# Kernel optimization log

Hardware: AMD Instinct MI355X
Metric: run time of the kernel (lower is better)

The kernel has to match this reference:

```python
import jax, jax.numpy as jnp
import numpy as np

B, S, E, H, DK, DV = 2, 2048, 1024, 16, 64, 64
NEG = -1e9


def setup_inputs() -> dict:
    key = jax.random.key(0)
    ks = jax.random.split(key, 12)
    s = 0.02
    return {
        "query": jax.random.normal(ks[0], (B, S, E), jnp.float32),
        "key": jax.random.normal(ks[1], (B, S, E), jnp.float32),
        "value": jax.random.normal(ks[2], (B, S, E), jnp.float32),
        "mask": jax.random.randint(ks[3], (B, S, S), 0, 2, jnp.int32),
        "Wq": jax.random.normal(ks[4], (E, H * DK), jnp.float32) * s,
        "bq": jnp.zeros((H * DK,), jnp.float32),
        "Wk": jax.random.normal(ks[5], (E, H * DK), jnp.float32) * s,
        "bk": jnp.zeros((H * DK,), jnp.float32),
        "Wv": jax.random.normal(ks[6], (E, H * DV), jnp.float32) * s,
        "bv": jnp.zeros((H * DV,), jnp.float32),
        "Wo": jax.random.normal(ks[7], (H * DV, E), jnp.float32) * s,
        "bo": jnp.zeros((E,), jnp.float32),
    }


def reference(query, key, value, mask, Wq, bq, Wk, bk, Wv, bv, Wo, bo):
    # projections, then split heads: (B,S,H*D) -> (B,H,S,D)
    q = (query @ Wq + bq).reshape(B, S, H, DK).transpose(0, 2, 1, 3)
    k = (key @ Wk + bk).reshape(B, S, H, DK).transpose(0, 2, 1, 3)
    v = (value @ Wv + bv).reshape(B, S, H, DV).transpose(0, 2, 1, 3)
    scores = jnp.einsum("bhqd,bhkd->bhqk", q, k) / jnp.sqrt(jnp.float32(DK))
    scores = jnp.where(mask[:, None, :, :] == 0, jnp.float32(NEG), scores)
    weights = jax.nn.softmax(scores, axis=-1)
    ctx = jnp.einsum("bhqk,bhkd->bhqd", weights, v)
    ctx = ctx.transpose(0, 2, 1, 3).reshape(B, S, H * DV)
    return ctx @ Wo + bo
```

## Files before the change

kernel.cpp:

```cpp
#include <hip/hip_runtime.h>

typedef __attribute__((ext_vector_type(8))) short s16x8;
typedef __attribute__((ext_vector_type(4))) float f32x4;
typedef unsigned short u16;
typedef unsigned int u32;
typedef unsigned long long u64;

__device__ __forceinline__ u16 f2bf(float f) {
  u32 u = __builtin_bit_cast(u32, f);
  u += 0x7fff + ((u >> 16) & 1);
  return (u16)(u >> 16);
}

__device__ __forceinline__ float exp2fast(float x) {
#if __has_builtin(__builtin_amdgcn_exp2f)
  return __builtin_amdgcn_exp2f(x);
#else
  return __expf(x * 0.6931471805599453f);
#endif
}

__device__ __forceinline__ void gload16(const void* g, void* l) {
  __builtin_amdgcn_global_load_lds((const __attribute__((address_space(1))) u32*)g,
                                   (__attribute__((address_space(3))) u32*)l, 16, 0, 0);
}

#define MFMA(a, b, c) __builtin_amdgcn_mfma_f32_16x16x32_bf16((a), (b), (c), 0, 0, 0)

#define QSCALE 0.18033688011112042f

__global__ __launch_bounds__(256) void cvt_bf16_3(const float* __restrict__ q,
                                                  const float* __restrict__ k,
                                                  const float* __restrict__ v,
                                                  u16* __restrict__ oq, u16* __restrict__ ok,
                                                  u16* __restrict__ ov) {
  int z = blockIdx.y;
  const float* src = (z == 0) ? q : (z == 1) ? k : v;
  u16* dst = (z == 0) ? oq : (z == 1) ? ok : ov;
  int i = blockIdx.x * 256 + threadIdx.x;
  const float4* s4 = (const float4*)src;
  float4 a = s4[2 * i], b = s4[2 * i + 1];
  uint4 o;
  o.x = (u32)f2bf(a.x) | ((u32)f2bf(a.y) << 16);
  o.y = (u32)f2bf(a.z) | ((u32)f2bf(a.w) << 16);
  o.z = (u32)f2bf(b.x) | ((u32)f2bf(b.y) << 16);
  o.w = (u32)f2bf(b.z) | ((u32)f2bf(b.w) << 16);
  ((uint4*)dst)[i] = o;
}

__global__ __launch_bounds__(256) void mask_bits(const int* __restrict__ mask,
                                                 u64* __restrict__ mb) {
  int wi = (blockIdx.x * 256 + threadIdx.x) >> 6;
  int lane = threadIdx.x & 63;
  u64 bits = __ballot(mask[((size_t)wi << 6) + lane] != 0);
  if (lane == 0) mb[wi] = bits;
}

__global__ __launch_bounds__(256) void transpose_w4(const float* __restrict__ W0,
                                                    const float* __restrict__ W1,
                                                    const float* __restrict__ W2,
                                                    const float* __restrict__ W3,
                                                    u16* __restrict__ T0, u16* __restrict__ T1,
                                                    u16* __restrict__ T2, u16* __restrict__ T3) {
  int z = blockIdx.z;
  const float* W = (z == 0) ? W0 : (z == 1) ? W1 : (z == 2) ? W2 : W3;
  u16* WT = (z == 0) ? T0 : (z == 1) ? T1 : (z == 2) ? T2 : T3;
  __shared__ float t[32][33];
  int tx = threadIdx.x, ty = threadIdx.y;
  int n = blockIdx.x * 32 + tx;
#pragma unroll
  for (int j = 0; j < 4; j++) {
    int k = blockIdx.y * 32 + ty + 8 * j;
    t[ty + 8 * j][tx] = W[(size_t)k * 1024 + n];
  }
  __syncthreads();
  int k = blockIdx.y * 32 + tx;
#pragma unroll
  for (int j = 0; j < 4; j++) {
    int n2 = blockIdx.x * 32 + ty + 8 * j;
    WT[(size_t)n2 * 1024 + k] = f2bf(t[tx][ty + 8 * j]);
  }
}

template <int BM, int BN>
__device__ __forceinline__ void gemm_core(const u16* __restrict__ A, const u16* __restrict__ BT,
                                          int m0, int n0, u16* Ash, u16* Bsh,
                                          f32x4 (&acc)[BM / 32][BN / 32]) {
  constexpr int MF = BM / 32, NF = BN / 32;
  constexpr int BATCH = BM / 32 + BN / 32;
  const int tid = threadIdx.x;
  const int lane = tid & 63, wid = tid >> 6;
  const int r16 = lane & 15, g = lane >> 4;
  const int wm = wid >> 1, wn = wid & 1;
  const int swz = r16 & 7;
  const f32x4 vz = {0.f, 0.f, 0.f, 0.f};
#pragma unroll
  for (int mf = 0; mf < MF; mf++)
#pragma unroll
    for (int nf = 0; nf < NF; nf++) acc[mf][nf] = vz;

  auto stage = [&](int buf, int k0) {
#pragma unroll
    for (int i = 0; i < MF; i++) {
      int ch = i * 256 + tid;
      int row = ch >> 3, sc = (ch & 7) ^ (row & 7);
      gload16(A + (((size_t)(m0 + row)) << 10) + k0 + sc * 8,
              Ash + (size_t)buf * (BM * 64) + ch * 8);
    }
#pragma unroll
    for (int i = 0; i < NF; i++) {
      int ch = i * 256 + tid;
      int row = ch >> 3, sc = (ch & 7) ^ (row & 7);
      gload16(BT + (((size_t)(n0 + row)) << 10) + k0 + sc * 8,
              Bsh + (size_t)buf * (BN * 64) + ch * 8);
    }
  };

  asm volatile("" ::: "memory");
  stage(0, 0);
  asm volatile("" ::: "memory");
  stage(1, 64);
  asm volatile("" ::: "memory");

  for (int t = 0; t < 16; t++) {
    const int cur = t & 1;
    if (t == 15) {
      asm volatile("s_waitcnt vmcnt(0)" ::: "memory");
    } else if constexpr (BATCH == 8) {
      asm volatile("s_waitcnt vmcnt(8)" ::: "memory");
    } else {
      asm volatile("s_waitcnt vmcnt(6)" ::: "memory");
    }
    asm volatile("s_barrier" ::: "memory");

    const u16* Acur = Ash + (size_t)cur * (BM * 64);
    const u16* Bcur = Bsh + (size_t)cur * (BN * 64);
    __builtin_amdgcn_s_setprio(1);
#pragma unroll
    for (int kk = 0; kk < 2; kk++) {
      const int c = (kk * 4 + g);
      s16x8 af[MF], bfr[NF];
#pragma unroll
      for (int mf = 0; mf < MF; mf++)
        af[mf] = *(const s16x8*)(Acur + ((wm * (BM / 2) + mf * 16 + r16) << 6) +
                                 ((c ^ swz) << 3));
#pragma unroll
      for (int nf = 0; nf < NF; nf++)
        bfr[nf] = *(const s16x8*)(Bcur + ((wn * (BN / 2) + nf * 16 + r16) << 6) +
                                  ((c ^ swz) << 3));
#pragma unroll
      for (int mf = 0; mf < MF; mf++)
#pragma unroll
        for (int nf = 0; nf < NF; nf++) acc[mf][nf] = MFMA(af[mf], bfr[nf], acc[mf][nf]);
    }
    __builtin_amdgcn_s_setprio(0);

    asm volatile("s_barrier" ::: "memory");
    if (t + 2 < 16) stage(cur, (t + 2) * 64);
  }
}

__global__ __launch_bounds__(256, 2) void proj_gemm(
    const u16* __restrict__ Xq, const u16* __restrict__ Xk, const u16* __restrict__ Xv,
    const u16* __restrict__ WqT, const u16* __restrict__ WkT, const u16* __restrict__ WvT,
    const float* __restrict__ bq, const float* __restrict__ bk, const float* __restrict__ bv,
    u16* __restrict__ Qo, u16* __restrict__ Ko, u16* __restrict__ Vto) {
  __shared__ u16 Ash[2 * 128 * 64], Bsh[2 * 128 * 64];
  const int z = blockIdx.z;
  const u16* A = (z == 0) ? Xq : (z == 1) ? Xk : Xv;
  const u16* BT = (z == 0) ? WqT : (z == 1) ? WkT : WvT;
  const float* bias = (z == 0) ? bq : (z == 1) ? bk : bv;
  u16* O = (z == 0) ? Qo : (z == 1) ? Ko : Vto;
  const float sc = (z == 0) ? QSCALE : 1.0f;
  const int m0 = blockIdx.y * 128, n0 = blockIdx.x * 128;
  f32x4 acc[4][4];
  gemm_core<128, 128>(A, BT, m0, n0, Ash, Bsh, acc);
  const int tid = threadIdx.x, lane = tid & 63, wid = tid >> 6;
  const int r16 = lane & 15, g = lane >> 4, wm = wid >> 1, wn = wid & 1;
#pragma unroll
  for (int nf = 0; nf < 4; nf++) {
    int col = n0 + wn * 64 + nf * 16 + r16;
    float bb = bias[col];
    int h = col >> 6, d = col & 63;
#pragma unroll
    for (int mf = 0; mf < 4; mf++) {
#pragma unroll
      for (int ri = 0; ri < 4; ri++) {
        int row = m0 + wm * 64 + mf * 16 + g * 4 + ri;
        int b_ = row >> 11, s_ = row & 2047;
        u16 val = f2bf((acc[mf][nf][ri] + bb) * sc);
        if (z < 2)
          O[((((size_t)b_ * 16 + h) * 2048 + s_) << 6) + d] = val;
        else
          O[((((size_t)b_ * 16 + h) * 64 + d) << 11) + s_] = val;
      }
    }
  }
}

__global__ __launch_bounds__(256, 2) void out_gemm(const u16* __restrict__ ctx,
                                                   const u16* __restrict__ WoT,
                                                   const float* __restrict__ bo,
                                                   float* __restrict__ out) {
  __shared__ u16 Ash[2 * 64 * 64], Bsh[2 * 128 * 64];
  const int m0 = blockIdx.y * 64, n0 = blockIdx.x * 128;
  f32x4 acc[2][4];
  gemm_core<64, 128>(ctx, WoT, m0, n0, Ash, Bsh, acc);
  const int tid = threadIdx.x, lane = tid & 63, wid = tid >> 6;
  const int r16 = lane & 15, g = lane >> 4, wm = wid >> 1, wn = wid & 1;
#pragma unroll
  for (int nf = 0; nf < 4; nf++) {
    int col = n0 + wn * 64 + nf * 16 + r16;
    float bb = bo[col];
#pragma unroll
    for (int mf = 0; mf < 2; mf++) {
#pragma unroll
      for (int ri = 0; ri < 4; ri++) {
        int row = m0 + wm * 32 + mf * 16 + g * 4 + ri;
        out[((size_t)row << 10) + col] = acc[mf][nf][ri] + bb;
      }
    }
  }
}

__global__ __launch_bounds__(256, 2) void flash_attn(const u16* __restrict__ Q,
                                                     const u16* __restrict__ K,
                                                     const u16* __restrict__ Vt,
                                                     const u64* __restrict__ Mb64,
                                                     u16* __restrict__ ctx) {
  __shared__ __align__(16) u16 Ksh[2][64][64];
  __shared__ __align__(16) u16 Vsh[2][64][64];
  __shared__ __align__(16) u16 P[4][32][72];

  const int tid = threadIdx.x, w = tid >> 6, lane = tid & 63;
  const int r16 = lane & 15, g = lane >> 4;
  const int b = blockIdx.z, h = blockIdx.y;
  const int q0 = blockIdx.x * 128 + w * 32;
  const u16* Qb = Q + ((size_t)(b * 16 + h) << 17);
  const u16* Kb = K + ((size_t)(b * 16 + h) << 17);
  const u16* Vb = Vt + ((size_t)(b * 16 + h) << 17);
  const u64* Mrow0 = Mb64 + ((size_t)(b * 2048 + q0 + r16) << 5);
  const u64* Mrow1 = Mb64 + ((size_t)(b * 2048 + q0 + 16 + r16) << 5);
  u16* Pw = &P[w][0][0];

  const int srow = tid >> 3, sk16 = tid & 7;
#define STAGE(buf, kv0)                                                                   \
  {                                                                                       \
    _Pragma("unroll") for (int i = 0; i < 2; i++) {                                       \
      int row = i * 32 + srow;                                                            \
      int sc = sk16 ^ (row & 7);                                                          \
      gload16(Kb + (((size_t)((kv0) + row)) << 6) + sc * 8,                               \
              (char*)&Ksh[buf][0][0] + (i * 256 + tid) * 16);                             \
      gload16(Vb + (((size_t)row) << 11) + (kv0) + sc * 8,                                \
              (char*)&Vsh[buf][0][0] + (i * 256 + tid) * 16);                             \
    }                                                                                     \
  }

  s16x8 aq[2][2];
#pragma unroll
  for (int qb = 0; qb < 2; qb++)
#pragma unroll
    for (int c = 0; c < 2; c++)
      aq[qb][c] = *(const s16x8*)(Qb + ((q0 + qb * 16 + r16) << 6) + c * 32 + g * 8);
  asm volatile("" ::: "memory");
  STAGE(0, 0);
  u64 mcur0 = Mrow0[0], mcur1 = Mrow1[0];
  asm volatile("" ::: "memory");
  STAGE(1, 64);
  u64 mnext0 = Mrow0[1], mnext1 = Mrow1[1];
  asm volatile("" ::: "memory");

  s16x8 vones;
#pragma unroll
  for (int j = 0; j < 8; j++) vones[j] = (short)0x3F80;

  const f32x4 vz = {0.f, 0.f, 0.f, 0.f};
  f32x4 o[2][4], o4[2];
#pragma unroll
  for (int qb = 0; qb < 2; qb++) {
    o4[qb] = vz;
#pragma unroll
    for (int i = 0; i < 4; i++) o[qb][i] = vz;
  }

  for (int t = 0; t < 32; t++) {
    const int cur = t & 1;
    if (t == 31) {
      asm volatile("s_waitcnt vmcnt(0)" ::: "memory");
    } else {
      asm volatile("s_waitcnt vmcnt(6)" ::: "memory");
    }
    asm volatile("s_barrier" ::: "memory");

    f32x4 s_[2][4];
#pragma unroll
    for (int qb = 0; qb < 2; qb++)
#pragma unroll
      for (int nt = 0; nt < 4; nt++) s_[qb][nt] = vz;
    __builtin_amdgcn_s_setprio(1);
#pragma unroll
    for (int c = 0; c < 2; c++) {
#pragma unroll
      for (int nt = 0; nt < 4; nt++) {
        s16x8 ak = *(const s16x8*)((char*)&Ksh[cur][0][0] + (nt * 16 + r16) * 128 +
                                   (((c * 4 + g) ^ (r16 & 7)) << 4));
        s_[0][nt] = MFMA(ak, aq[0][c], s_[0][nt]);
        s_[1][nt] = MFMA(ak, aq[1][c], s_[1][nt]);
      }
    }
    __builtin_amdgcn_s_setprio(0);

#pragma unroll
    for (int qb = 0; qb < 2; qb++) {
      u64 m = ((qb == 0) ? mcur0 : mcur1) >> (g * 4);
      u32 mlo = (u32)m, mhi = (u32)(m >> 32);
#pragma unroll
      for (int nt = 0; nt < 4; nt++) {
        u32 word = (nt < 2) ? mlo : mhi;
        u32 sh = (nt & 1) << 4;
        float e0 = exp2fast(s_[qb][nt][0]) * (float)((word >> (sh + 0)) & 1);
        float e1 = exp2fast(s_[qb][nt][1]) * (float)((word >> (sh + 1)) & 1);
        float e2 = exp2fast(s_[qb][nt][2]) * (float)((word >> (sh + 2)) & 1);
        float e3 = exp2fast(s_[qb][nt][3]) * (float)((word >> (sh + 3)) & 1);
        u32 pk0, pk1;
        asm("v_cvt_pk_bf16_f32 %0, %1, %2" : "=v"(pk0) : "v"(e0), "v"(e1));
        asm("v_cvt_pk_bf16_f32 %0, %1, %2" : "=v"(pk1) : "v"(e2), "v"(e3));
        uint2 pr; pr.x = pk0; pr.y = pk1;
        *(uint2*)((char*)Pw + (qb * 16 + r16) * 144 + nt * 32 + g * 8) = pr;
      }
    }
    asm volatile("" ::: "memory");

    __builtin_amdgcn_s_setprio(1);
#pragma unroll
    for (int c = 0; c < 2; c++) {
      s16x8 pa0 = *(const s16x8*)((char*)Pw + r16 * 144 + c * 64 + g * 16);
      s16x8 pa1 = *(const s16x8*)((char*)Pw + (16 + r16) * 144 + c * 64 + g * 16);
#pragma unroll
      for (int nt = 0; nt < 4; nt++) {
        s16x8 bv = *(const s16x8*)((char*)&Vsh[cur][0][0] + (nt * 16 + r16) * 128 +
                                   (((c * 4 + g) ^ (r16 & 7)) << 4));
        o[0][nt] = MFMA(pa0, bv, o[0][nt]);
        o[1][nt] = MFMA(pa1, bv, o[1][nt]);
      }
      o4[0] = MFMA(pa0, vones, o4[0]);
      o4[1] = MFMA(pa1, vones, o4[1]);
    }
    __builtin_amdgcn_s_setprio(0);

    asm volatile("s_barrier" ::: "memory");
    u64 mnew0 = 0, mnew1 = 0;
    if (t + 2 < 32) {
      STAGE(cur, (t + 2) * 64);
      mnew0 = Mrow0[t + 2];
      mnew1 = Mrow1[t + 2];
    }
    mcur0 = mnext0; mcur1 = mnext1;
    mnext0 = mnew0; mnext1 = mnew1;
  }
#undef STAGE

#pragma unroll
  for (int qb = 0; qb < 2; qb++) {
    float invq[4];
#pragma unroll
    for (int ri = 0; ri < 4; ri++) invq[ri] = 1.f / o4[qb][ri];
#pragma unroll
    for (int nt = 0; nt < 4; nt++) {
      int col = (h << 6) + nt * 16 + r16;
#pragma unroll
      for (int ri = 0; ri < 4; ri++) {
        int row = (b << 11) + q0 + qb * 16 + g * 4 + ri;
        ctx[((size_t)row << 10) + col] = f2bf(o[qb][nt][ri] * invq[ri]);
      }
    }
  }
}

extern "C" void kernel_launch(void* const* d_in, const int* in_sizes, int n_in,
                              void* d_out, int out_size, void* d_ws, size_t ws_size,
                              hipStream_t stream) {
  const float* query = (const float*)d_in[0];
  const float* key_  = (const float*)d_in[1];
  const float* value = (const float*)d_in[2];
  const int*   mask  = (const int*)d_in[3];
  const float* Wq = (const float*)d_in[4];
  const float* bq = (const float*)d_in[5];
  const float* Wk = (const float*)d_in[6];
  const float* bk = (const float*)d_in[7];
  const float* Wv = (const float*)d_in[8];
  const float* bv = (const float*)d_in[9];
  const float* Wo = (const float*)d_in[10];
  const float* bo = (const float*)d_in[11];

  const size_t MB = 1048576;
  char* ws = (char*)d_ws;
  u16* Xq  = (u16*)(ws + 0 * MB);
  u16* Xk  = (u16*)(ws + 8 * MB);
  u16* Xv  = (u16*)(ws + 16 * MB);
  u16* WqT = (u16*)(ws + 24 * MB);
  u16* WkT = (u16*)(ws + 26 * MB);
  u16* WvT = (u16*)(ws + 28 * MB);
  u16* WoT = (u16*)(ws + 30 * MB);
  u16* Qd  = (u16*)(ws + 32 * MB);
  u16* Kd  = (u16*)(ws + 40 * MB);
  u16* Vtd = (u16*)(ws + 48 * MB);
  u16* ctx = (u16*)(ws + 56 * MB);
  u64* Mb  = (u64*)(ws + 72 * MB);

  cvt_bf16_3<<<dim3(2048, 3), 256, 0, stream>>>(query, key_, value, Xq, Xk, Xv);
  mask_bits<<<32768, 256, 0, stream>>>(mask, Mb);

  dim3 tb(32, 8);
  transpose_w4<<<dim3(32, 32, 4), tb, 0, stream>>>(Wq, Wk, Wv, Wo, WqT, WkT, WvT, WoT);

  proj_gemm<<<dim3(8, 32, 3), 256, 0, stream>>>(Xq, Xk, Xv, WqT, WkT, WvT, bq, bk, bv,
                                                Qd, Kd, Vtd);
  flash_attn<<<dim3(16, 16, 2), 256, 0, stream>>>(Qd, Kd, Vtd, Mb, ctx);
  out_gemm<<<dim3(8, 64), 256, 0, stream>>>(ctx, WoT, bo, (float*)d_out);
}
```

Before: 159.0 us.

## Switch flash attention to 32x32 MFMA with register-resident P via permlane swap

The flash attention kernel moves from 16x16x32 to 32x32x16 bf16 MFMAs, so the S=K·Q^T output layout can be repacked into the A-operand layout for P·V using v_permlane32_swap. This removes the per-tile LDS round trip for the probability matrix P and its shared buffer. The mask is now read with one u64 per lane instead of two, and the vmcnt wait is adjusted to match. The grid is flattened to 1D with a block swizzle so that blocks sharing a batch-head are spread in a different order, which may change L2 locality for K/V. The risk is higher register pressure from the 16-wide accumulators and correctness that depends on exact lane-layout matching.

Result: no change. 157.4 us (-1.0%).

```diff
diff --git a/kernel.cpp b/kernel.cpp
--- a/kernel.cpp
+++ b/kernel.cpp
@@ -2,6 +2,7 @@
 
 typedef __attribute__((ext_vector_type(8))) short s16x8;
 typedef __attribute__((ext_vector_type(4))) float f32x4;
+typedef __attribute__((ext_vector_type(16))) float f32x16;
 typedef unsigned short u16;
 typedef unsigned int u32;
 typedef unsigned long long u64;
@@ -26,6 +27,7 @@
 }
 
 #define MFMA(a, b, c) __builtin_amdgcn_mfma_f32_16x16x32_bf16((a), (b), (c), 0, 0, 0)
+#define MFMA32(a, b, c) __builtin_amdgcn_mfma_f32_32x32x16_bf16((a), (b), (c), 0, 0, 0)
 
 #define QSCALE 0.18033688011112042f
 
@@ -223,6 +225,33 @@
   }
 }
 
+__device__ __forceinline__ s16x8 pack4u(u32 a0, u32 a1, u32 b0, u32 b1) {
+  union { u32 u[4]; s16x8 v; } p;
+  p.u[0] = a0; p.u[1] = a1; p.u[2] = b0; p.u[3] = b1;
+  return p.v;
+}
+
+__device__ __forceinline__ void softpack(const f32x16& sv, u32 wm, s16x8& pA, s16x8& pB) {
+  float e[16];
+#pragma unroll
+  for (int qd = 0; qd < 4; qd++)
+#pragma unroll
+    for (int j = 0; j < 4; j++)
+      e[qd * 4 + j] = exp2fast(sv[qd * 4 + j]) * (float)((wm >> (qd * 8 + j)) & 1);
+#pragma unroll
+  for (int n = 0; n < 2; n++) {
+    u32 a0, a1, b0, b1;
+    asm("v_cvt_pk_bf16_f32 %0, %1, %2" : "=v"(a0) : "v"(e[n * 8 + 0]), "v"(e[n * 8 + 1]));
+    asm("v_cvt_pk_bf16_f32 %0, %1, %2" : "=v"(a1) : "v"(e[n * 8 + 2]), "v"(e[n * 8 + 3]));
+    asm("v_cvt_pk_bf16_f32 %0, %1, %2" : "=v"(b0) : "v"(e[n * 8 + 4]), "v"(e[n * 8 + 5]));
+    asm("v_cvt_pk_bf16_f32 %0, %1, %2" : "=v"(b1) : "v"(e[n * 8 + 6]), "v"(e[n * 8 + 7]));
+    asm("v_permlane32_swap_b32 %0, %1" : "+v"(a0), "+v"(b0));
+    asm("v_permlane32_swap_b32 %0, %1" : "+v"(a1), "+v"(b1));
+    if (n == 0) pA = pack4u(a0, a1, b0, b1);
+    else        pB = pack4u(a0, a1, b0, b1);
+  }
+}
+
 __global__ __launch_bounds__(256, 2) void flash_attn(const u16* __restrict__ Q,
                                                      const u16* __restrict__ K,
                                                      const u16* __restrict__ Vt,
@@ -230,18 +259,19 @@
                                                      u16* __restrict__ ctx) {
   __shared__ __align__(16) u16 Ksh[2][64][64];
   __shared__ __align__(16) u16 Vsh[2][64][64];
-  __shared__ __align__(16) u16 P[4][32][72];
 
   const int tid = threadIdx.x, w = tid >> 6, lane = tid & 63;
-  const int r16 = lane & 15, g = lane >> 4;
-  const int b = blockIdx.z, h = blockIdx.y;
-  const int q0 = blockIdx.x * 128 + w * 32;
-  const u16* Qb = Q + ((size_t)(b * 16 + h) << 17);
-  const u16* Kb = K + ((size_t)(b * 16 + h) << 17);
-  const u16* Vb = Vt + ((size_t)(b * 16 + h) << 17);
-  const u64* Mrow0 = Mb64 + ((size_t)(b * 2048 + q0 + r16) << 5);
-  const u64* Mrow1 = Mb64 + ((size_t)(b * 2048 + q0 + 16 + r16) << 5);
-  u16* Pw = &P[w][0][0];
+  const int l31 = lane & 31, h5 = lane >> 5, l7 = lane & 7;
+
+  int work = ((int)blockIdx.x & 7) * 64 + ((int)blockIdx.x >> 3);
+  const int qt = work & 15, bh = work >> 4;
+  const int b = bh >> 4, h = bh & 15;
+  const int q0 = qt * 128 + w * 32;
+
+  const u16* Qb = Q + ((size_t)bh << 17);
+  const u16* Kb = K + ((size_t)bh << 17);
+  const u16* Vb = Vt + ((size_t)bh << 17);
+  const u64* Mrow = Mb64 + ((size_t)(b * 2048 + q0 + l31) << 5);
 
   const int srow = tid >> 3, sk16 = tid & 7;
 #define STAGE(buf, kv0)                                                                   \
@@ -256,124 +286,87 @@
     }                                                                                     \
   }
 
-  s16x8 aq[2][2];
-#pragma unroll
-  for (int qb = 0; qb < 2; qb++)
-#pragma unroll
-    for (int c = 0; c < 2; c++)
-      aq[qb][c] = *(const s16x8*)(Qb + ((q0 + qb * 16 + r16) << 6) + c * 32 + g * 8);
+  s16x8 aq[4];
+#pragma unroll
+  for (int dk = 0; dk < 4; dk++)
+    aq[dk] = *(const s16x8*)(Qb + ((q0 + l31) << 6) + dk * 16 + h5 * 8);
   asm volatile("" ::: "memory");
   STAGE(0, 0);
-  u64 mcur0 = Mrow0[0], mcur1 = Mrow1[0];
+  u64 mcur = Mrow[0];
   asm volatile("" ::: "memory");
   STAGE(1, 64);
-  u64 mnext0 = Mrow0[1], mnext1 = Mrow1[1];
+  u64 mnext = Mrow[1];
   asm volatile("" ::: "memory");
 
   s16x8 vones;
 #pragma unroll
   for (int j = 0; j < 8; j++) vones[j] = (short)0x3F80;
 
-  const f32x4 vz = {0.f, 0.f, 0.f, 0.f};
-  f32x4 o[2][4], o4[2];
-#pragma unroll
-  for (int qb = 0; qb < 2; qb++) {
-    o4[qb] = vz;
-#pragma unroll
-    for (int i = 0; i < 4; i++) o[qb][i] = vz;
-  }
+  f32x16 o0, o1, o4;
+#pragma unroll
+  for (int r = 0; r < 16; r++) { o0[r] = 0.f; o1[r] = 0.f; o4[r] = 0.f; }
 
   for (int t = 0; t < 32; t++) {
     const int cur = t & 1;
     if (t == 31) {
       asm volatile("s_waitcnt vmcnt(0)" ::: "memory");
     } else {
-      asm volatile("s_waitcnt vmcnt(6)" ::: "memory");
+      asm volatile("s_waitcnt vmcnt(5)" ::: "memory");
     }
     asm volatile("s_barrier" ::: "memory");
 
-    f32x4 s_[2][4];
-#pragma unroll
-    for (int qb = 0; qb < 2; qb++)
-#pragma unroll
-      for (int nt = 0; nt < 4; nt++) s_[qb][nt] = vz;
+    const u16* Kc = &Ksh[cur][0][0];
+    const u16* Vc = &Vsh[cur][0][0];
+
+    f32x16 s0, s1;
+#pragma unroll
+    for (int r = 0; r < 16; r++) { s0[r] = 0.f; s1[r] = 0.f; }
     __builtin_amdgcn_s_setprio(1);
 #pragma unroll
-    for (int c = 0; c < 2; c++) {
-#pragma unroll
-      for (int nt = 0; nt < 4; nt++) {
-        s16x8 ak = *(const s16x8*)((char*)&Ksh[cur][0][0] + (nt * 16 + r16) * 128 +
-                                   (((c * 4 + g) ^ (r16 & 7)) << 4));
-        s_[0][nt] = MFMA(ak, aq[0][c], s_[0][nt]);
-        s_[1][nt] = MFMA(ak, aq[1][c], s_[1][nt]);
-      }
+    for (int dk = 0; dk < 4; dk++) {
+      int ch = (((dk << 1) + h5) ^ l7) << 3;
+      s16x8 ak0 = *(const s16x8*)(Kc + (l31 << 6) + ch);
+      s16x8 ak1 = *(const s16x8*)(Kc + ((32 + l31) << 6) + ch);
+      s0 = MFMA32(ak0, aq[dk], s0);
+      s1 = MFMA32(ak1, aq[dk], s1);
     }
     __builtin_amdgcn_s_setprio(0);
 
-#pragma unroll
-    for (int qb = 0; qb < 2; qb++) {
-      u64 m = ((qb == 0) ? mcur0 : mcur1) >> (g * 4);
-      u32 mlo = (u32)m, mhi = (u32)(m >> 32);
-#pragma unroll
-      for (int nt = 0; nt < 4; nt++) {
-        u32 word = (nt < 2) ? mlo : mhi;
-        u32 sh = (nt & 1) << 4;
-        float e0 = exp2fast(s_[qb][nt][0]) * (float)((word >> (sh + 0)) & 1);
-        float e1 = exp2fast(s_[qb][nt][1]) * (float)((word >> (sh + 1)) & 1);
-        float e2 = exp2fast(s_[qb][nt][2]) * (float)((word >> (sh + 2)) & 1);
-        float e3 = exp2fast(s_[qb][nt][3]) * (float)((word >> (sh + 3)) & 1);
-        u32 pk0, pk1;
-        asm("v_cvt_pk_bf16_f32 %0, %1, %2" : "=v"(pk0) : "v"(e0), "v"(e1));
-        asm("v_cvt_pk_bf16_f32 %0, %1, %2" : "=v"(pk1) : "v"(e2), "v"(e3));
-        uint2 pr; pr.x = pk0; pr.y = pk1;
-        *(uint2*)((char*)Pw + (qb * 16 + r16) * 144 + nt * 32 + g * 8) = pr;
-      }
-    }
-    asm volatile("" ::: "memory");
+    u64 msh = mcur >> (h5 << 2);
+    s16x8 pa[4];
+    softpack(s0, (u32)msh, pa[0], pa[1]);
+    softpack(s1, (u32)(msh >> 32), pa[2], pa[3]);
 
     __builtin_amdgcn_s_setprio(1);
 #pragma unroll
-    for (int c = 0; c < 2; c++) {
-      s16x8 pa0 = *(const s16x8*)((char*)Pw + r16 * 144 + c * 64 + g * 16);
-      s16x8 pa1 = *(const s16x8*)((char*)Pw + (16 + r16) * 144 + c * 64 + g * 16);
-#pragma unroll
-      for (int nt = 0; nt < 4; nt++) {
-        s16x8 bv = *(const s16x8*)((char*)&Vsh[cur][0][0] + (nt * 16 + r16) * 128 +
-                                   (((c * 4 + g) ^ (r16 & 7)) << 4));
-        o[0][nt] = MFMA(pa0, bv, o[0][nt]);
-        o[1][nt] = MFMA(pa1, bv, o[1][nt]);
-      }
-      o4[0] = MFMA(pa0, vones, o4[0]);
-      o4[1] = MFMA(pa1, vones, o4[1]);
+    for (int km = 0; km < 4; km++) {
+      int ch = (((km << 1) + h5) ^ l7) << 3;
+      s16x8 bv0 = *(const s16x8*)(Vc + (l31 << 6) + ch);
+      s16x8 bv1 = *(const s16x8*)(Vc + ((32 + l31) << 6) + ch);
+      o0 = MFMA32(pa[km], bv0, o0);
+      o1 = MFMA32(pa[km], bv1, o1);
+      o4 = MFMA32(pa[km], vones, o4);
     }
     __builtin_amdgcn_s_setprio(0);
 
     asm volatile("s_barrier" ::: "memory");
-    u64 mnew0 = 0, mnew1 = 0;
+    u64 mnew = 0;
     if (t + 2 < 32) {
       STAGE(cur, (t + 2) * 64);
-      mnew0 = Mrow0[t + 2];
-      mnew1 = Mrow1[t + 2];
-    }
-    mcur0 = mnext0; mcur1 = mnext1;
-    mnext0 = mnew0; mnext1 = mnew1;
+      mnew = Mrow[t + 2];
+    }
+    mcur = mnext;
+    mnext = mnew;
   }
 #undef STAGE
 
 #pragma unroll
-  for (int qb = 0; qb < 2; qb++) {
-    float invq[4];
-#pragma unroll
-    for (int ri = 0; ri < 4; ri++) invq[ri] = 1.f / o4[qb][ri];
-#pragma unroll
-    for (int nt = 0; nt < 4; nt++) {
-      int col = (h << 6) + nt * 16 + r16;
-#pragma unroll
-      for (int ri = 0; ri < 4; ri++) {
-        int row = (b << 11) + q0 + qb * 16 + g * 4 + ri;
-        ctx[((size_t)row << 10) + col] = f2bf(o[qb][nt][ri] * invq[ri]);
-      }
-    }
+  for (int r = 0; r < 16; r++) {
+    int qr = (r & 3) + 8 * (r >> 2) + 4 * h5;
+    size_t rowoff = ((size_t)((b << 11) + q0 + qr)) << 10;
+    float iv = 1.f / o4[r];
+    ctx[rowoff + (h << 6) + l31]      = f2bf(o0[r] * iv);
+    ctx[rowoff + (h << 6) + 32 + l31] = f2bf(o1[r] * iv);
   }
 }
 
@@ -416,6 +409,6 @@
 
   proj_gemm<<<dim3(8, 32, 3), 256, 0, stream>>>(Xq, Xk, Xv, WqT, WkT, WvT, bq, bk, bv,
                                                 Qd, Kd, Vtd);
-  flash_attn<<<dim3(16, 16, 2), 256, 0, stream>>>(Qd, Kd, Vtd, Mb, ctx);
+  flash_attn<<<512, 256, 0, stream>>>(Qd, Kd, Vtd, Mb, ctx);
   out_gemm<<<dim3(8, 64), 256, 0, stream>>>(ctx, WoT, bo, (float*)d_out);
 }
```
